# Kernel optimization log

Hardware: AMD Instinct MI355X
Metric: run time of the kernel (lower is better)

Reference implementation:

```python
import jax, jax.numpy as jnp
import numpy as np

N_NODES = 100000
N_EDGES = 1600000


def _deg_norm(idx, n):
    deg = jax.ops.segment_sum(jnp.ones(idx.shape[0], jnp.float32), idx, num_segments=n)
    return jnp.where(deg > 0, jax.lax.rsqrt(jnp.maximum(deg, 1.0)), 0.0)


def gcn_layer(src, dst, x, W, b):
    # DGL GraphConv, norm='both': D_in^{-1/2} A D_out^{-1/2} X W + b
    n = x.shape[0]
    h = x @ W                                   # project first (in >= out)
    norm_src = _deg_norm(src, n)                # out-degree norm at source
    norm_dst = _deg_norm(dst, n)                # in-degree norm at destination
    msg = (h * norm_src[:, None])[src]          # [E, d] gather
    agg = jax.ops.segment_sum(msg, dst, num_segments=n)
    return agg * norm_dst[:, None] + b


def setup_inputs() -> dict:
    key = jax.random.key(0)
    ks = jax.random.split(key, 6)
    in_f, h_f, n_cls = 256, 128, 64
    feat = jax.random.normal(ks[0], (N_NODES, in_f), jnp.float32)
    src = jax.random.randint(ks[1], (N_EDGES,), 0, N_NODES, jnp.int32)
    dst = jax.random.randint(ks[2], (N_EDGES,), 0, N_NODES, jnp.int32)
    W1 = jax.random.normal(ks[3], (in_f, h_f), jnp.float32) / np.sqrt(in_f)
    b1 = jnp.zeros((h_f,), jnp.float32)
    W2 = jax.random.normal(ks[4], (h_f, n_cls), jnp.float32) / np.sqrt(h_f)
    b2 = jnp.zeros((n_cls,), jnp.float32)
    return {"feat": feat, "src": src, "dst": dst, "W1": W1, "b1": b1, "W2": W2, "b2": b2}


def reference(feat, src, dst, W1, b1, W2, b2):
    h = gcn_layer(src, dst, feat, W1, b1)
    h = jax.nn.relu(h)
    h = gcn_layer(src, dst, h, W2, b2)
    return jax.nn.sigmoid(h)
```

## Files before the change

### kernel.cpp

```cpp
#include <hip/hip_runtime.h>
#include <cmath>

#define IN_F 256
#define H_F  128
#define N_CLS 64
#define SCAN_CHUNK 2048
#define EPB 4096
#define MAXBK 400

typedef __attribute__((ext_vector_type(8))) short bf16x8;
typedef __attribute__((ext_vector_type(4))) float f32x4;

__device__ __forceinline__ ushort f2bf(float x) {
  unsigned b = __builtin_bit_cast(unsigned, x);
  b += 0x7FFF + ((b >> 16) & 1);
  return (ushort)(b >> 16);
}

__global__ __launch_bounds__(256) void hist_conv_kernel(
    const int* __restrict__ src, const int* __restrict__ dst, int* __restrict__ hist,
    const float* __restrict__ W1, ushort* __restrict__ W1T,
    const float* __restrict__ W2, ushort* __restrict__ W2T,
    int NBK, int NBLK, int E) {
  int blk = blockIdx.x, t = threadIdx.x;
  if (blk >= NBLK) {
    int i = (blk - NBLK) * 256 + t;
    if (i < IN_F * H_F) {
      int k = i / H_F, n = i % H_F;
      W1T[n * IN_F + k] = f2bf(W1[i]);
    } else if (i < IN_F * H_F + H_F * N_CLS) {
      int j = i - IN_F * H_F;
      int k = j / N_CLS, n = j % N_CLS;
      W2T[n * H_F + k] = f2bf(W2[j]);
    }
    return;
  }
  __shared__ int hD[MAXBK], hS[MAXBK];
  for (int b = t; b < NBK; b += 256) { hD[b] = 0; hS[b] = 0; }
  __syncthreads();
  int e0 = blk * EPB;
#pragma unroll
  for (int j = 0; j < EPB / 256; ++j) {
    int idx = e0 + j * 256 + t;
    if (idx < E) {
      atomicAdd(&hD[dst[idx] >> 8], 1);
      atomicAdd(&hS[src[idx] >> 8], 1);
    }
  }
  __syncthreads();
  for (int b = t; b < NBK; b += 256) {
    hist[(size_t)b * NBLK + blk] = hD[b];
    hist[(size_t)(NBK + b) * NBLK + blk] = hS[b];
  }
}

__device__ void excl_scan_lds(int* cnt, int* pos, int t, int nbk) {
  for (int b = t; b < nbk; b += 256) pos[b] = cnt[b];
  __syncthreads();
  for (int d = 1; d < 256; d <<= 1) {
    int u = (t < nbk && t >= d) ? pos[t - d] : 0;
    __syncthreads();
    if (t < nbk && t >= d) pos[t] += u;
    __syncthreads();
  }
  int m2 = nbk - 256;
  int s0 = (m2 > 0) ? pos[255] : 0;
  for (int d = 1; d < 256; d <<= 1) {
    int u = (m2 > 0 && t < m2 && t >= d) ? pos[256 + t - d] : 0;
    __syncthreads();
    if (m2 > 0 && t < m2 && t >= d) pos[256 + t] += u;
    __syncthreads();
  }
  if (m2 > 0 && t < m2) pos[256 + t] += s0;
  __syncthreads();
  for (int b = t; b < nbk; b += 256) pos[b] -= cnt[b];
  __syncthreads();
}

__global__ __launch_bounds__(256) void scatter_kernel(const int* __restrict__ src,
                                                      const int* __restrict__ dst,
                                                      const int* __restrict__ P,
                                                      int* __restrict__ pairs_pk,
                                                      int* __restrict__ srcs_s,
                                                      int NBK, int NBLK, int E) {
  __shared__ int cnt[MAXBK], pos[MAXBK], cur[MAXBK], gb[MAXBK];
  __shared__ int stage_pk[EPB];
  __shared__ ushort stage_b[EPB];
  int t = threadIdx.x, blk = blockIdx.x;
  int e0 = blk * EPB;
  int ne = E - e0; if (ne > EPB) ne = EPB;

  for (int b = t; b < NBK; b += 256) cnt[b] = 0;
  __syncthreads();
#pragma unroll
  for (int j = 0; j < EPB / 256; ++j) {
    int idx = e0 + j * 256 + t;
    if (idx < E) atomicAdd(&cnt[dst[idx] >> 8], 1);
  }
  __syncthreads();
  excl_scan_lds(cnt, pos, t, NBK);
  for (int b = t; b < NBK; b += 256) { cur[b] = pos[b]; gb[b] = P[(size_t)b * NBLK + blk]; }
  __syncthreads();
#pragma unroll
  for (int j = 0; j < EPB / 256; ++j) {
    int idx = e0 + j * 256 + t;
    if (idx < E) {
      int d = dst[idx];
      int r = atomicAdd(&cur[d >> 8], 1);
      stage_pk[r] = (src[idx] << 8) | (d & 255);
      stage_b[r] = (ushort)(d >> 8);
    }
  }
  __syncthreads();
  for (int i = t; i < ne; i += 256) {
    int b = stage_b[i];
    pairs_pk[gb[b] + (i - pos[b])] = stage_pk[i];
  }
  __syncthreads();

  for (int b = t; b < NBK; b += 256) cnt[b] = 0;
  __syncthreads();
#pragma unroll
  for (int j = 0; j < EPB / 256; ++j) {
    int idx = e0 + j * 256 + t;
    if (idx < E) atomicAdd(&cnt[src[idx] >> 8], 1);
  }
  __syncthreads();
  excl_scan_lds(cnt, pos, t, NBK);
  for (int b = t; b < NBK; b += 256) {
    cur[b] = pos[b];
    gb[b] = P[(size_t)(NBK + b) * NBLK + blk] - E;
  }
  __syncthreads();
#pragma unroll
  for (int j = 0; j < EPB / 256; ++j) {
    int idx = e0 + j * 256 + t;
    if (idx < E) {
      int s = src[idx];
      int r = atomicAdd(&cur[s >> 8], 1);
      stage_pk[r] = s;
    }
  }
  __syncthreads();
  for (int i = t; i < ne; i += 256) {
    int s = stage_pk[i];
    int b = s >> 8;
    srcs_s[gb[b] + (i - pos[b])] = s;
  }
}

__global__ __launch_bounds__(256) void csr_outdeg_bucket(
    const int* __restrict__ pairs_pk, const int* __restrict__ srcs_s,
    const int* __restrict__ P, int* __restrict__ row_off,
    float* __restrict__ norm_d, float* __restrict__ norm_s,
    int* __restrict__ csr, int NBK, int NBLK, int N, int E) {
  __shared__ int cnt[256], pos[256], cur[256];
  int b = blockIdx.x, t = threadIdx.x;
  int node = b * 256 + t;

  int bstart = P[(size_t)b * NBLK];
  int bend = (b + 1 < NBK) ? P[(size_t)(b + 1) * NBLK] : E;
  cnt[t] = 0;
  __syncthreads();
  for (int i = bstart + t; i < bend; i += 256) atomicAdd(&cnt[pairs_pk[i] & 255], 1);
  __syncthreads();
  pos[t] = cnt[t];
  __syncthreads();
  for (int d = 1; d < 256; d <<= 1) {
    int u = (t >= d) ? pos[t - d] : 0;
    __syncthreads();
    if (t >= d) pos[t] += u;
    __syncthreads();
  }
  int excl = pos[t] - cnt[t];
  if (node < N) {
    row_off[node] = bstart + excl;
    norm_d[node] = cnt[t] > 0 ? rsqrtf((float)cnt[t]) : 0.f;
  }
  if (b == NBK - 1 && t == 255) row_off[N] = E;
  cur[t] = excl;
  __syncthreads();
  for (int i = bstart + t; i < bend; i += 256) {
    int pk = pairs_pk[i];
    int r = atomicAdd(&cur[pk & 255], 1);
    csr[bstart + r] = (int)((unsigned)pk >> 8);
  }
  __syncthreads();

  size_t SOFF = (size_t)NBK * NBLK;
  int sstart = P[SOFF + (size_t)b * NBLK] - E;
  int send = (b + 1 < NBK) ? P[SOFF + (size_t)(b + 1) * NBLK] - E : E;
  cnt[t] = 0;
  __syncthreads();
  for (int i = sstart + t; i < send; i += 256) atomicAdd(&cnt[srcs_s[i] & 255], 1);
  __syncthreads();
  if (node < N) norm_s[node] = cnt[t] > 0 ? rsqrtf((float)cnt[t]) : 0.f;
}

__global__ void scan_part(const int* __restrict__ arr, int* __restrict__ bsum, int len) {
  int base = blockIdx.x * SCAN_CHUNK + threadIdx.x * 8;
  int s = 0;
#pragma unroll
  for (int j = 0; j < 8; ++j) {
    int i = base + j;
    if (i < len) s += arr[i];
  }
#pragma unroll
  for (int d = 1; d < 64; d <<= 1) s += __shfl_xor(s, d);
  __shared__ int ws[4];
  int lane = threadIdx.x & 63, w = threadIdx.x >> 6;
  if (lane == 0) ws[w] = s;
  __syncthreads();
  if (threadIdx.x == 0) bsum[blockIdx.x] = ws[0] + ws[1] + ws[2] + ws[3];
}

__global__ __launch_bounds__(1024) void scan_bsum(int* __restrict__ bsum, int nb) {
  __shared__ int sm[1024];
  int t = threadIdx.x;
  sm[t] = (t < nb) ? bsum[t] : 0;
  __syncthreads();
  for (int d = 1; d < 1024; d <<= 1) {
    int v = (t >= d) ? sm[t - d] : 0;
    __syncthreads();
    sm[t] += v;
    __syncthreads();
  }
  if (t < nb) bsum[t] = (t == 0) ? 0 : sm[t - 1];
}

__global__ void scan_final(const int* __restrict__ arr, const int* __restrict__ bsum_ex,
                           int* __restrict__ outp, int len, int total) {
  int base = blockIdx.x * SCAN_CHUNK + threadIdx.x * 8;
  int v[8], pre[8];
  int s = 0;
#pragma unroll
  for (int j = 0; j < 8; ++j) {
    int i = base + j;
    v[j] = (i < len) ? arr[i] : 0;
    pre[j] = s;
    s += v[j];
  }
  int lane = threadIdx.x & 63, w = threadIdx.x >> 6;
  int inc = s;
#pragma unroll
  for (int d = 1; d < 64; d <<= 1) {
    int u = __shfl_up(inc, d);
    if (lane >= d) inc += u;
  }
  __shared__ int wsum[4], woff[4];
  if (lane == 63) wsum[w] = inc;
  __syncthreads();
  if (threadIdx.x == 0) {
    int r = 0;
    for (int q = 0; q < 4; ++q) { woff[q] = r; r += wsum[q]; }
  }
  __syncthreads();
  int ex = (inc - s) + woff[w] + bsum_ex[blockIdx.x];
#pragma unroll
  for (int j = 0; j < 8; ++j) {
    int i = base + j;
    if (i < len) outp[i] = ex + pre[j];
  }
  if (blockIdx.x == 0 && threadIdx.x == 0) outp[len] = total;
}

__global__ __launch_bounds__(256) void mfma_gemm1(
    const float* __restrict__ A, const ushort* __restrict__ BT,
    const float* __restrict__ scale, ushort* __restrict__ C, int M) {
  constexpr int BM = 128, BN = 128, KTOT = 256, BK = 64, WM = 2, WN = 2;
  constexpr int FM = (BM / WM) / 16;
  constexpr int FN = (BN / WN) / 16;
  constexpr int ABYTES = BM * BK * 2;
  constexpr int BBYTES = BN * BK * 2;
  __shared__ char lds[ABYTES + BBYTES];
  char* Asm = lds;
  char* Bsm = lds + ABYTES;

  const int tid = threadIdx.x;
  const int lane = tid & 63;
  const int w = tid >> 6;
  const int wm = w / WN, wn = w % WN;
  const int m0 = blockIdx.x * BM;

  f32x4 acc[FM][FN];
#pragma unroll
  for (int m = 0; m < FM; ++m)
#pragma unroll
    for (int n = 0; n < FN; ++n) acc[m][n] = (f32x4){0.f, 0.f, 0.f, 0.f};

  const int ra = lane & 15;
  const int kg = lane >> 4;

  float4 pfa[8];
#pragma unroll
  for (int s = 0; s < 4; ++s) {
    int L = s * 4096 + tid * 16;
    int r = L >> 7;
    int slot = (L >> 4) & 7;
    int gr = m0 + r; if (gr >= M) gr = M - 1;
    const float4* gp = (const float4*)(A + (size_t)gr * KTOT + slot * 8);
    pfa[2 * s] = gp[0];
    pfa[2 * s + 1] = gp[1];
  }

  for (int kt = 0; kt < KTOT / BK; ++kt) {
#pragma unroll
    for (int s = 0; s < 4; ++s) {
      int L = s * 4096 + tid * 16;
      int r = L >> 7;
      float4 va = pfa[2 * s], vb = pfa[2 * s + 1];
      bf16x8 o;
      o[0] = (short)f2bf(va.x); o[1] = (short)f2bf(va.y);
      o[2] = (short)f2bf(va.z); o[3] = (short)f2bf(va.w);
      o[4] = (short)f2bf(vb.x); o[5] = (short)f2bf(vb.y);
      o[6] = (short)f2bf(vb.z); o[7] = (short)f2bf(vb.w);
      *(bf16x8*)(Asm + (L ^ ((r & 7) << 4))) = o;
    }
#pragma unroll
    for (int s = 0; s < BBYTES / 4096; ++s) {
      int L = s * 4096 + tid * 16;
      int r = L >> 7;
      int slot = (L >> 4) & 7;
      const char* gp = (const char*)BT + (size_t)r * (KTOT * 2) + kt * (BK * 2)
                     + ((slot * 16) ^ ((r & 7) << 4));
      __builtin_amdgcn_global_load_lds(
          (const __attribute__((address_space(1))) unsigned*)gp,
          (__attribute__((address_space(3))) unsigned*)(Bsm + L), 16, 0, 0);
    }
    if (kt + 1 < KTOT / BK) {
#pragma unroll
      for (int s = 0; s < 4; ++s) {
        int L = s * 4096 + tid * 16;
        int r = L >> 7;
        int slot = (L >> 4) & 7;
        int gr = m0 + r; if (gr >= M) gr = M - 1;
        const float4* gp = (const float4*)(A + (size_t)gr * KTOT + (kt + 1) * BK + slot * 8);
        pfa[2 * s] = gp[0];
        pfa[2 * s + 1] = gp[1];
      }
    }
    __syncthreads();

#pragma unroll
    for (int ks = 0; ks < 2; ++ks) {
      bf16x8 af[FM], bfr[FN];
#pragma unroll
      for (int m = 0; m < FM; ++m) {
        int r = wm * (BM / WM) + m * 16 + ra;
        int cb = ks * 64 + kg * 16;
        af[m] = *(const bf16x8*)(Asm + r * 128 + (cb ^ ((r & 7) << 4)));
      }
#pragma unroll
      for (int n = 0; n < FN; ++n) {
        int c = wn * (BN / WN) + n * 16 + ra;
        int cb = ks * 64 + kg * 16;
        bfr[n] = *(const bf16x8*)(Bsm + c * 128 + (cb ^ ((c & 7) << 4)));
      }
#pragma unroll
      for (int m = 0; m < FM; ++m)
#pragma unroll
        for (int n = 0; n < FN; ++n)
          acc[m][n] = __builtin_amdgcn_mfma_f32_16x16x32_bf16(af[m], bfr[n], acc[m][n], 0, 0, 0);
    }
    __syncthreads();
  }

#pragma unroll
  for (int m = 0; m < FM; ++m) {
#pragma unroll
    for (int j = 0; j < 4; ++j) {
      int rl = wm * (BM / WM) + m * 16 + (lane >> 4) * 4 + j;
      int gr = m0 + rl;
      if (gr < M) {
        float sc = scale[gr];
#pragma unroll
        for (int n = 0; n < FN; ++n) {
          int c = wn * (BN / WN) + n * 16 + (lane & 15);
          C[(size_t)gr * BN + c] = f2bf(acc[m][n][j] * sc);
        }
      }
    }
  }
}

template<int BM, int BN, int KTOT, int WM, int WN>
__global__ __launch_bounds__(256) void mfma_gemm_scale(
    const ushort* __restrict__ A, const ushort* __restrict__ BT,
    const float* __restrict__ scale, ushort* __restrict__ C, int M) {
  constexpr int BK = 64;
  constexpr int FM = (BM / WM) / 16;
  constexpr int FN = (BN / WN) / 16;
  constexpr int ABYTES = BM * BK * 2;
  constexpr int BBYTES = BN * BK * 2;
  __shared__ char lds[ABYTES + BBYTES];
  char* Asm = lds;
  char* Bsm = lds + ABYTES;

  const int tid = threadIdx.x;
  const int lane = tid & 63;
  const int w = tid >> 6;
  const int wm = w / WN, wn = w % WN;
  const int m0 = blockIdx.x * BM;

  f32x4 acc[FM][FN];
#pragma unroll
  for (int m = 0; m < FM; ++m)
#pragma unroll
    for (int n = 0; n < FN; ++n) acc[m][n] = (f32x4){0.f, 0.f, 0.f, 0.f};

  const int ra = lane & 15;
  const int kg = lane >> 4;

  for (int kt = 0; kt < KTOT / BK; ++kt) {
#pragma unroll
    for (int s = 0; s < ABYTES / 4096; ++s) {
      int L = s * 4096 + tid * 16;
      int r = L >> 7;
      int slot = (L >> 4) & 7;
      int gr = m0 + r; if (gr >= M) gr = M - 1;
      const char* gp = (const char*)A + (size_t)gr * (KTOT * 2) + kt * (BK * 2)
                     + ((slot * 16) ^ ((r & 7) << 4));
      __builtin_amdgcn_global_load_lds(
          (const __attribute__((address_space(1))) unsigned*)gp,
          (__attribute__((address_space(3))) unsigned*)(Asm + L), 16, 0, 0);
    }
#pragma unroll
    for (int s = 0; s < BBYTES / 4096; ++s) {
      int L = s * 4096 + tid * 16;
      int r = L >> 7;
      int slot = (L >> 4) & 7;
      const char* gp = (const char*)BT + (size_t)r * (KTOT * 2) + kt * (BK * 2)
                     + ((slot * 16) ^ ((r & 7) << 4));
      __builtin_amdgcn_global_load_lds(
          (const __attribute__((address_space(1))) unsigned*)gp,
          (__attribute__((address_space(3))) unsigned*)(Bsm + L), 16, 0, 0);
    }
    __syncthreads();

#pragma unroll
    for (int ks = 0; ks < 2; ++ks) {
      bf16x8 af[FM], bfr[FN];
#pragma unroll
      for (int m = 0; m < FM; ++m) {
        int r = wm * (BM / WM) + m * 16 + ra;
        int cb = ks * 64 + kg * 16;
        af[m] = *(const bf16x8*)(Asm + r * 128 + (cb ^ ((r & 7) << 4)));
      }
#pragma unroll
      for (int n = 0; n < FN; ++n) {
        int c = wn * (BN / WN) + n * 16 + ra;
        int cb = ks * 64 + kg * 16;
        bfr[n] = *(const bf16x8*)(Bsm + c * 128 + (cb ^ ((c & 7) << 4)));
      }
#pragma unroll
      for (int m = 0; m < FM; ++m)
#pragma unroll
        for (int n = 0; n < FN; ++n)
          acc[m][n] = __builtin_amdgcn_mfma_f32_16x16x32_bf16(af[m], bfr[n], acc[m][n], 0, 0, 0);
    }
    __syncthreads();
  }

#pragma unroll
  for (int m = 0; m < FM; ++m) {
#pragma unroll
    for (int j = 0; j < 4; ++j) {
      int rl = wm * (BM / WM) + m * 16 + (lane >> 4) * 4 + j;
      int gr = m0 + rl;
      if (gr < M) {
        float sc = scale[gr];
#pragma unroll
        for (int n = 0; n < FN; ++n) {
          int c = wn * (BN / WN) + n * 16 + (lane & 15);
          C[(size_t)gr * BN + c] = f2bf(acc[m][n][j] * sc);
        }
      }
    }
  }
}

__global__ void gather1(const ushort* __restrict__ h1, const int* __restrict__ off,
                        const int* __restrict__ csr, const float* __restrict__ nd,
                        const float* __restrict__ b1, ushort* __restrict__ x2, int N) {
  int w = (blockIdx.x * blockDim.x + threadIdx.x) >> 6;
  int lane = threadIdx.x & 63;
  if (w >= N) return;
  int lo = off[w], hi = off[w + 1];
  const unsigned* h = (const unsigned*)h1;
  float sx = 0.f, sy = 0.f;
#define ACC1(u) { sx += __builtin_bit_cast(float, (u) << 16); \
                  sy += __builtin_bit_cast(float, (u) & 0xFFFF0000u); }
  int j = lo;
  for (; j + 16 <= hi; j += 16) {
    int s0 = csr[j+0], s1 = csr[j+1], s2 = csr[j+2], s3 = csr[j+3];
    int s4 = csr[j+4], s5 = csr[j+5], s6 = csr[j+6], s7 = csr[j+7];
    int s8 = csr[j+8], s9 = csr[j+9], sa = csr[j+10], sb = csr[j+11];
    int sc_ = csr[j+12], sd = csr[j+13], se = csr[j+14], sf = csr[j+15];
    unsigned u0 = h[(size_t)s0 * 64 + lane];
    unsigned u1 = h[(size_t)s1 * 64 + lane];
    unsigned u2 = h[(size_t)s2 * 64 + lane];
    unsigned u3 = h[(size_t)s3 * 64 + lane];
    unsigned u4 = h[(size_t)s4 * 64 + lane];
    unsigned u5 = h[(size_t)s5 * 64 + lane];
    unsigned u6 = h[(size_t)s6 * 64 + lane];
    unsigned u7 = h[(size_t)s7 * 64 + lane];
    unsigned u8 = h[(size_t)s8 * 64 + lane];
    unsigned u9 = h[(size_t)s9 * 64 + lane];
    unsigned ua = h[(size_t)sa * 64 + lane];
    unsigned ub = h[(size_t)sb * 64 + lane];
    unsigned uc = h[(size_t)sc_ * 64 + lane];
    unsigned ud = h[(size_t)sd * 64 + lane];
    unsigned ue = h[(size_t)se * 64 + lane];
    unsigned uf = h[(size_t)sf * 64 + lane];
    ACC1(u0) ACC1(u1) ACC1(u2) ACC1(u3) ACC1(u4) ACC1(u5) ACC1(u6) ACC1(u7)
    ACC1(u8) ACC1(u9) ACC1(ua) ACC1(ub) ACC1(uc) ACC1(ud) ACC1(ue) ACC1(uf)
  }
  for (; j + 4 <= hi; j += 4) {
    int s0 = csr[j+0], s1 = csr[j+1], s2 = csr[j+2], s3 = csr[j+3];
    unsigned u0 = h[(size_t)s0 * 64 + lane];
    unsigned u1 = h[(size_t)s1 * 64 + lane];
    unsigned u2 = h[(size_t)s2 * 64 + lane];
    unsigned u3 = h[(size_t)s3 * 64 + lane];
    ACC1(u0) ACC1(u1) ACC1(u2) ACC1(u3)
  }
  for (; j < hi; ++j) {
    int s = csr[j];
    unsigned u = h[(size_t)s * 64 + lane];
    ACC1(u)
  }
#undef ACC1
  float sc = nd[w];
  float2 bb = ((const float2*)b1)[lane];
  float ox = fmaxf(sx * sc + bb.x, 0.f);
  float oy = fmaxf(sy * sc + bb.y, 0.f);
  ushort2 o; o.x = f2bf(ox); o.y = f2bf(oy);
  ((ushort2*)x2)[(size_t)w * 64 + lane] = o;
}

__global__ void gather2(const ushort* __restrict__ h2, const int* __restrict__ off,
                        const int* __restrict__ csr, const float* __restrict__ nd,
                        const float* __restrict__ b2, float* __restrict__ out, int N) {
  int wv = (blockIdx.x * blockDim.x + threadIdx.x) >> 6;
  int lane = threadIdx.x & 63;
  int grp = lane >> 5;
  int sub = lane & 31;
  int node = wv * 2 + grp;
  if (node >= N) return;
  int lo = off[node], hi = off[node + 1];
  const unsigned* h = (const unsigned*)h2;
  float s0f = 0.f, s1f = 0.f;
#define ACC2(u) { s0f += __builtin_bit_cast(float, (u) << 16); \
                  s1f += __builtin_bit_cast(float, (u) & 0xFFFF0000u); }
  int j = lo;
  for (; j + 16 <= hi; j += 16) {
    int i0 = csr[j+0], i1 = csr[j+1], i2 = csr[j+2], i3 = csr[j+3];
    int i4 = csr[j+4], i5 = csr[j+5], i6 = csr[j+6], i7 = csr[j+7];
    int i8 = csr[j+8], i9 = csr[j+9], ia = csr[j+10], ib = csr[j+11];
    int ic = csr[j+12], id = csr[j+13], ie = csr[j+14], if_ = csr[j+15];
    unsigned u0 = h[(size_t)i0 * 32 + sub];
    unsigned u1 = h[(size_t)i1 * 32 + sub];
    unsigned u2 = h[(size_t)i2 * 32 + sub];
    unsigned u3 = h[(size_t)i3 * 32 + sub];
    unsigned u4 = h[(size_t)i4 * 32 + sub];
    unsigned u5 = h[(size_t)i5 * 32 + sub];
    unsigned u6 = h[(size_t)i6 * 32 + sub];
    unsigned u7 = h[(size_t)i7 * 32 + sub];
    unsigned u8 = h[(size_t)i8 * 32 + sub];
    unsigned u9 = h[(size_t)i9 * 32 + sub];
    unsigned ua = h[(size_t)ia * 32 + sub];
    unsigned ub = h[(size_t)ib * 32 + sub];
    unsigned uc = h[(size_t)ic * 32 + sub];
    unsigned ud = h[(size_t)id * 32 + sub];
    unsigned ue = h[(size_t)ie * 32 + sub];
    unsigned uf = h[(size_t)if_ * 32 + sub];
    ACC2(u0) ACC2(u1) ACC2(u2) ACC2(u3) ACC2(u4) ACC2(u5) ACC2(u6) ACC2(u7)
    ACC2(u8) ACC2(u9) ACC2(ua) ACC2(ub) ACC2(uc) ACC2(ud) ACC2(ue) ACC2(uf)
  }
  for (; j + 4 <= hi; j += 4) {
    int i0 = csr[j+0], i1 = csr[j+1], i2 = csr[j+2], i3 = csr[j+3];
    unsigned u0 = h[(size_t)i0 * 32 + sub];
    unsigned u1 = h[(size_t)i1 * 32 + sub];
    unsigned u2 = h[(size_t)i2 * 32 + sub];
    unsigned u3 = h[(size_t)i3 * 32 + sub];
    ACC2(u0) ACC2(u1) ACC2(u2) ACC2(u3)
  }
  for (; j < hi; ++j) {
    int i0 = csr[j];
    unsigned u = h[(size_t)i0 * 32 + sub];
    ACC2(u)
  }
#undef ACC2
  float scn = nd[node];
  float2 bb = ((const float2*)b2)[sub];
  float v0 = s0f * scn + bb.x;
  float v1 = s1f * scn + bb.y;
  float2 o;
  o.x = 1.f / (1.f + expf(-v0));
  o.y = 1.f / (1.f + expf(-v1));
  ((float2*)out)[(size_t)node * 32 + sub] = o;
}

extern "C" void kernel_launch(void* const* d_in, const int* in_sizes, int n_in,
                              void* d_out, int out_size, void* d_ws, size_t ws_size,
                              hipStream_t stream) {
  const float* feat = (const float*)d_in[0];
  const int*   src  = (const int*)d_in[1];
  const int*   dst  = (const int*)d_in[2];
  const float* W1   = (const float*)d_in[3];
  const float* b1   = (const float*)d_in[4];
  const float* W2   = (const float*)d_in[5];
  const float* b2   = (const float*)d_in[6];
  float* out = (float*)d_out;

  const int N = in_sizes[0] / IN_F;
  const int E = in_sizes[1];

  const int NBK  = (N + 255) >> 8;
  const int NBLK = (E + EPB - 1) / EPB;
  const int HLEN = 2 * NBK * NBLK;
  const int WBLK = (IN_F * H_F + H_F * N_CLS + 255) / 256;

  size_t off = 0;
  auto alloc = [&](size_t bytes) -> void* {
    void* p = (char*)d_ws + off;
    off = (off + bytes + 255) & ~(size_t)255;
    return p;
  };
  int*    hist    = (int*)alloc((size_t)HLEN * 4);
  int*    P       = (int*)alloc((size_t)(HLEN + 1) * 4);
  int*    bsum    = (int*)alloc((size_t)1024 * 4);
  int*    pairs_pk= (int*)alloc((size_t)E * 4);
  int*    srcs_s  = (int*)alloc((size_t)E * 4);
  float*  norm_s  = (float*)alloc((size_t)N * 4);
  float*  norm_d  = (float*)alloc((size_t)N * 4);
  int*    row_off = (int*)alloc((size_t)(N + 1) * 4);
  int*    csr     = (int*)alloc((size_t)E * 4);
  ushort* w1t     = (ushort*)alloc((size_t)H_F * IN_F * 2);
  ushort* w2t     = (ushort*)alloc((size_t)N_CLS * H_F * 2);
  ushort* h1      = (ushort*)alloc((size_t)N * H_F * 2);
  ushort* x2bf    = (ushort*)alloc((size_t)N * H_F * 2);
  ushort* h2      = (ushort*)alloc((size_t)N * N_CLS * 2);
  (void)ws_size;

  hist_conv_kernel<<<NBLK + WBLK, 256, 0, stream>>>(src, dst, hist, W1, w1t, W2, w2t,
                                                    NBK, NBLK, E);
  const int NBS = (HLEN + SCAN_CHUNK - 1) / SCAN_CHUNK;
  scan_part<<<NBS, 256, 0, stream>>>(hist, bsum, HLEN);
  scan_bsum<<<1, 1024, 0, stream>>>(bsum, NBS);
  scan_final<<<NBS, 256, 0, stream>>>(hist, bsum, P, HLEN, 2 * E);
  scatter_kernel<<<NBLK, 256, 0, stream>>>(src, dst, P, pairs_pk, srcs_s, NBK, NBLK, E);
  csr_outdeg_bucket<<<NBK, 256, 0, stream>>>(pairs_pk, srcs_s, P, row_off,
                                             norm_d, norm_s, csr, NBK, NBLK, N, E);

  mfma_gemm1<<<(N + 127) / 128, 256, 0, stream>>>(feat, w1t, norm_s, h1, N);
  gather1<<<(N * 64 + 255) / 256, 256, 0, stream>>>(h1, row_off, csr, norm_d, b1, x2bf, N);

  mfma_gemm_scale<128, 64, 128, 2, 2><<<(N + 127) / 128, 256, 0, stream>>>(
      x2bf, w2t, norm_s, h2, N);
  int pairs = (N + 1) / 2;
  gather2<<<(pairs * 64 + 255) / 256, 256, 0, stream>>>(h2, row_off, csr, norm_d, b2, out, N);
}
```

Measured before the change: 215.1 us.

## Replace LDS barrier scans with wave-shuffle scans and halve edges per block

The exclusive scans in scatter_kernel and csr_outdeg_bucket used Hillis-Steele passes over LDS with two barriers per step. They are replaced by intra-wavefront __shfl_up scans plus a small cross-wave total, which cuts barrier count. EPB is also halved from 4096 to 2048, which doubles the number of partition blocks (more parallelism, smaller per-block LDS staging) but enlarges the histogram/prefix table P and the number of per-block bucket writes. The new scan handles up to 512 buckets with two elements per thread. MAXBK stays at 400.

```diff
diff --git a/kernel.cpp b/kernel.cpp
--- a/kernel.cpp
+++ b/kernel.cpp
@@ -5,7 +5,7 @@
 #define H_F  128
 #define N_CLS 64
 #define SCAN_CHUNK 2048
-#define EPB 4096
+#define EPB 2048
 #define MAXBK 400
 
 typedef __attribute__((ext_vector_type(8))) short bf16x8;
@@ -54,26 +54,27 @@
   }
 }
 
-__device__ void excl_scan_lds(int* cnt, int* pos, int t, int nbk) {
-  for (int b = t; b < nbk; b += 256) pos[b] = cnt[b];
-  __syncthreads();
-  for (int d = 1; d < 256; d <<= 1) {
-    int u = (t < nbk && t >= d) ? pos[t - d] : 0;
-    __syncthreads();
-    if (t < nbk && t >= d) pos[t] += u;
-    __syncthreads();
-  }
-  int m2 = nbk - 256;
-  int s0 = (m2 > 0) ? pos[255] : 0;
-  for (int d = 1; d < 256; d <<= 1) {
-    int u = (m2 > 0 && t < m2 && t >= d) ? pos[256 + t - d] : 0;
-    __syncthreads();
-    if (m2 > 0 && t < m2 && t >= d) pos[256 + t] += u;
-    __syncthreads();
-  }
-  if (m2 > 0 && t < m2) pos[256 + t] += s0;
-  __syncthreads();
-  for (int b = t; b < nbk; b += 256) pos[b] -= cnt[b];
+__device__ void excl_scan_wave(const int* cnt, int* pos, int t, int nbk) {
+  __shared__ int wtot[4];
+  int lane = t & 63, w = t >> 6;
+  int e0 = 2 * t, e1 = 2 * t + 1;
+  int a = (e0 < nbk) ? cnt[e0] : 0;
+  int b = (e1 < nbk) ? cnt[e1] : 0;
+  int s = a + b;
+  int inc = s;
+#pragma unroll
+  for (int d = 1; d < 64; d <<= 1) {
+    int u = __shfl_up(inc, d);
+    if (lane >= d) inc += u;
+  }
+  if (lane == 63) wtot[w] = inc;
+  __syncthreads();
+  int woff = 0;
+#pragma unroll
+  for (int q = 0; q < 4; ++q) woff += (q < w) ? wtot[q] : 0;
+  int ex = woff + inc - s;
+  if (e0 < nbk) pos[e0] = ex;
+  if (e1 < nbk) pos[e1] = ex + a;
   __syncthreads();
 }
 
@@ -98,7 +99,7 @@
     if (idx < E) atomicAdd(&cnt[dst[idx] >> 8], 1);
   }
   __syncthreads();
-  excl_scan_lds(cnt, pos, t, NBK);
+  excl_scan_wave(cnt, pos, t, NBK);
   for (int b = t; b < NBK; b += 256) { cur[b] = pos[b]; gb[b] = P[(size_t)b * NBLK + blk]; }
   __syncthreads();
 #pragma unroll
@@ -126,7 +127,7 @@
     if (idx < E) atomicAdd(&cnt[src[idx] >> 8], 1);
   }
   __syncthreads();
-  excl_scan_lds(cnt, pos, t, NBK);
+  excl_scan_wave(cnt, pos, t, NBK);
   for (int b = t; b < NBK; b += 256) {
     cur[b] = pos[b];
     gb[b] = P[(size_t)(NBK + b) * NBLK + blk] - E;
@@ -154,9 +155,10 @@
     const int* __restrict__ P, int* __restrict__ row_off,
     float* __restrict__ norm_d, float* __restrict__ norm_s,
     int* __restrict__ csr, int NBK, int NBLK, int N, int E) {
-  __shared__ int cnt[256], pos[256], cur[256];
+  __shared__ int cnt[256], cur[256], wtot[4];
   int b = blockIdx.x, t = threadIdx.x;
   int node = b * 256 + t;
+  int lane = t & 63, w = t >> 6;
 
   int bstart = P[(size_t)b * NBLK];
   int bend = (b + 1 < NBK) ? P[(size_t)(b + 1) * NBLK] : E;
@@ -164,18 +166,22 @@
   __syncthreads();
   for (int i = bstart + t; i < bend; i += 256) atomicAdd(&cnt[pairs_pk[i] & 255], 1);
   __syncthreads();
-  pos[t] = cnt[t];
-  __syncthreads();
-  for (int d = 1; d < 256; d <<= 1) {
-    int u = (t >= d) ? pos[t - d] : 0;
-    __syncthreads();
-    if (t >= d) pos[t] += u;
-    __syncthreads();
-  }
-  int excl = pos[t] - cnt[t];
+  int c = cnt[t];
+  int inc = c;
+#pragma unroll
+  for (int d = 1; d < 64; d <<= 1) {
+    int u = __shfl_up(inc, d);
+    if (lane >= d) inc += u;
+  }
+  if (lane == 63) wtot[w] = inc;
+  __syncthreads();
+  int woff = 0;
+#pragma unroll
+  for (int q = 0; q < 4; ++q) woff += (q < w) ? wtot[q] : 0;
+  int excl = woff + inc - c;
   if (node < N) {
     row_off[node] = bstart + excl;
-    norm_d[node] = cnt[t] > 0 ? rsqrtf((float)cnt[t]) : 0.f;
+    norm_d[node] = c > 0 ? rsqrtf((float)c) : 0.f;
   }
   if (b == NBK - 1 && t == 255) row_off[N] = E;
   cur[t] = excl;
```

Measured after the change: 214.8 us. Within noise of the previous version (-0.1%).
